# Kernel tuning notes

Hardware: AMD Instinct MI355X
Metric: run time of the kernel (lower is better)

Reference implementation:

```python
import jax, jax.numpy as jnp
import numpy as np

B, T, D, H, DK, DV = 2, 2048, 1024, 16, 64, 64
_MASK_ADDER = -10000.0  # tf-models MaskedSoftmax convention


def setup_inputs() -> dict:
    key = jax.random.key(0)
    ks = jax.random.split(key, 8)
    s = 0.02
    return {
        "query": jax.random.normal(ks[0], (B, T, D), jnp.float32),
        "value": jax.random.normal(ks[1], (B, T, D), jnp.float32),
        "Wq": jax.random.normal(ks[2], (D, H, DK), jnp.float32) * s,
        "bq": jnp.zeros((H, DK), jnp.float32),
        "Wk": jax.random.normal(ks[3], (D, H, DK), jnp.float32) * s,
        "bk": jnp.zeros((H, DK), jnp.float32),
        "Wv": jax.random.normal(ks[4], (D, H, DV), jnp.float32) * s,
        "bv": jnp.zeros((H, DV), jnp.float32),
        "Wo": jax.random.normal(ks[5], (H, DV, D), jnp.float32) * s,
        "bo": jnp.zeros((D,), jnp.float32),
        "attention_mask": jnp.ones((B, T, T), jnp.int32),
    }


def reference(query, value, Wq, bq, Wk, bk, Wv, bv, Wo, bo, attention_mask):
    # key defaults to value (call() with key=None); training=False -> no dropout
    q = jnp.einsum("btd,dhk->bthk", query, Wq) + bq          # [B,T,H,DK]
    k = jnp.einsum("bsd,dhk->bshk", value, Wk) + bk          # [B,S,H,DK]
    v = jnp.einsum("bsd,dhk->bshk", value, Wv) + bv          # [B,S,H,DV]
    q = q * (1.0 / jnp.sqrt(jnp.asarray(DK, q.dtype)))
    scores = jnp.einsum("bthk,bshk->bhts", q, k)             # [B,H,T,S]
    # MaskedSoftmax: expand mask at axis 1, additive -10000 on masked slots
    adder = (1.0 - attention_mask.astype(scores.dtype))[:, None, :, :] * _MASK_ADDER
    probs = jax.nn.softmax(scores + adder, axis=-1)
    ctx = jnp.einsum("bhts,bshv->bthv", probs, v)            # [B,T,H,DV]
    out = jnp.einsum("bthv,hvd->btd", ctx, Wo) + bo          # [B,T,D]
    return out
```

## Files before the change

kernel.cpp:

```cpp
#include <hip/hip_runtime.h>
#include <hip/hip_bf16.h>
#include <stdint.h>

#define TSEQ 2048
#define DMODEL 1024
#define NHEAD 16
#define HDIM 64
#define MROWS 4096
#define L2E 1.44269504088896340736f

typedef unsigned short u16;
typedef unsigned int u32;
typedef __attribute__((ext_vector_type(8))) short bf16x8;
typedef __attribute__((ext_vector_type(8))) unsigned short u16x8;
typedef __attribute__((ext_vector_type(4))) unsigned short u16x4;
typedef __attribute__((ext_vector_type(4))) float f32x4;
typedef __attribute__((ext_vector_type(16))) float f32x16;
typedef __attribute__((ext_vector_type(4))) unsigned int u32x4;

__device__ inline u16 f2bf(float f) {
  __hip_bfloat16 h(f);
  return __builtin_bit_cast(u16, h);
}

__device__ inline float fexp2(float x) { float r; asm("v_exp_f32 %0, %1" : "=v"(r) : "v"(x)); return r; }

__device__ inline unsigned cvtpk_bf16(float a, float b) {
  unsigned r; asm("v_cvt_pk_bf16_f32 %0, %1, %2" : "=v"(r) : "v"(a), "v"(b)); return r;
}

__device__ inline void permswap(u32& a, u32& b) {
  asm volatile("v_permlane32_swap_b32 %0, %1" : "+v"(a), "+v"(b));
}

__device__ inline void gload16(const void* g, void* l) {
  __builtin_amdgcn_global_load_lds((const __attribute__((address_space(1))) void*)g,
                                   (__attribute__((address_space(3))) void*)l, 16, 0, 0);
}

__global__ void prep(const float* __restrict__ q, const float* __restrict__ v,
                     u16* __restrict__ qo, u16* __restrict__ vo,
                     const float* __restrict__ Wq, const float* __restrict__ Wk,
                     const float* __restrict__ Wv, const float* __restrict__ Wo,
                     u16* __restrict__ WT3, u16* __restrict__ WoT,
                     const int* __restrict__ mask, int* __restrict__ flags) {
  __shared__ float tile[32][33];
  __shared__ int sred[4];
  const int bid = blockIdx.x, tid = threadIdx.x;
  if (bid < 8192) {
    const float* in = bid < 4096 ? q : v;
    u16* out = bid < 4096 ? qo : vo;
    const int i = (bid & 4095) * 1024 + tid * 4;
    float4 x = *(const float4*)(in + i);
    u16x4 o;
    o.x = f2bf(x.x); o.y = f2bf(x.y); o.z = f2bf(x.z); o.w = f2bf(x.w);
    *(u16x4*)(out + i) = o;
  } else if (bid < 12288) {
    int t = bid - 8192;
    const int z = t >> 10; t &= 1023;
    const float* W = z == 0 ? Wq : z == 1 ? Wk : z == 2 ? Wv : Wo;
    u16* WT = z < 3 ? (WT3 + (size_t)z * 1024 * 1024) : WoT;
    const int bx = t & 31, by = t >> 5;
    const int tr = tid >> 3;
    const int tc4 = (tid & 7) * 4;
    float4 x = *(const float4*)(W + (size_t)(by * 32 + tr) * 1024 + bx * 32 + tc4);
    tile[tr][tc4 + 0] = x.x; tile[tr][tc4 + 1] = x.y;
    tile[tr][tc4 + 2] = x.z; tile[tr][tc4 + 3] = x.w;
    __syncthreads();
    u16x4 o;
    o.x = f2bf(tile[tc4 + 0][tr]); o.y = f2bf(tile[tc4 + 1][tr]);
    o.z = f2bf(tile[tc4 + 2][tr]); o.w = f2bf(tile[tc4 + 3][tr]);
    *(u16x4*)(WT + (size_t)(bx * 32 + tr) * 1024 + by * 32 + tc4) = o;
  } else {
    const int t = bid - 12288;
    const int st = t & 15, qt = (t >> 4) & 15, b = t >> 8;
    const int row = qt * 128 + (tid >> 1);
    const int col0 = st * 128 + (tid & 1) * 64;
    const int* p = mask + (size_t)b * TSEQ * TSEQ + (size_t)row * TSEQ + col0;
    int ok = 1;
    #pragma unroll
    for (int j = 0; j < 64; j += 4) {
      int4 x = *(const int4*)(p + j);
      ok &= (x.x == 1) & (x.y == 1) & (x.z == 1) & (x.w == 1);
    }
    ok = __all(ok);
    if ((tid & 63) == 0) sred[tid >> 6] = ok;
    __syncthreads();
    if (tid == 0) flags[(b * 16 + qt) * 16 + st] = sred[0] & sred[1] & sred[2] & sred[3];
  }
}

__global__ __launch_bounds__(256) void gemm_qkv(
    const u16* __restrict__ qxb, const u16* __restrict__ vxb, const u16* __restrict__ WT3,
    const float* __restrict__ bq, const float* __restrict__ bk, const float* __restrict__ bv,
    u16* __restrict__ Qb, u16* __restrict__ Kb, u16* __restrict__ VTb, float qscale) {
  __shared__ u16 SMEM[64 * 64 + 128 * 64];
  u16* As = SMEM;
  u16* Bs = SMEM + 64 * 64;
  const int tid = threadIdx.x;
  const int w = tid >> 6, lane = tid & 63;
  const int lo = lane & 15, hi = lane >> 4;
  const int bid = blockIdx.x + (blockIdx.y << 6);
  const int swz = (bid & 7) * 192 + (bid >> 3);
  const int m0 = (swz & 63) << 6, n0 = (swz >> 6) << 7;
  const int nsel = n0 >> 10;
  const u16* A = nsel == 0 ? qxb : vxb;
  const float* bias = nsel == 0 ? bq : nsel == 1 ? bk : bv;
  const float scl = nsel == 0 ? qscale : 1.0f;
  const int wm = (w >> 1) * 32, wn = (w & 1) * 64;
  f32x4 acc[2][4] = {};
  for (int kt = 0; kt < 16; ++kt) {
    #pragma unroll
    for (int i = 0; i < 2; ++i) {
      const int off = tid * 16 + i * 4096;
      const int row = off >> 7;
      const int g = ((off >> 4) & 7) ^ (row & 7);
      gload16(A + (size_t)(m0 + row) * 1024 + kt * 64 + g * 8, (char*)As + off);
    }
    #pragma unroll
    for (int i = 0; i < 4; ++i) {
      const int off = tid * 16 + i * 4096;
      const int row = off >> 7;
      const int g = ((off >> 4) & 7) ^ (row & 7);
      gload16(WT3 + (size_t)(n0 + row) * 1024 + kt * 64 + g * 8, (char*)Bs + off);
    }
    __syncthreads();
    #pragma unroll
    for (int kk = 0; kk < 2; ++kk) {
      bf16x8 af[2], bfr[4];
      #pragma unroll
      for (int mi = 0; mi < 2; ++mi) {
        int row = wm + mi * 16 + lo;
        af[mi] = *(const bf16x8*)(As + row * 64 + (((kk * 4 + hi) ^ (row & 7)) << 3));
      }
      #pragma unroll
      for (int ni = 0; ni < 4; ++ni) {
        int row = wn + ni * 16 + lo;
        bfr[ni] = *(const bf16x8*)(Bs + row * 64 + (((kk * 4 + hi) ^ (row & 7)) << 3));
      }
      #pragma unroll
      for (int mi = 0; mi < 2; ++mi)
        #pragma unroll
        for (int ni = 0; ni < 4; ++ni)
          acc[mi][ni] = __builtin_amdgcn_mfma_f32_16x16x32_bf16(af[mi], bfr[ni], acc[mi][ni], 0, 0, 0);
    }
    __syncthreads();
  }
  if (nsel < 2) {
    u16* dst = nsel == 0 ? Qb : Kb;
    #pragma unroll
    for (int ni = 0; ni < 4; ++ni) {
      const int col = (n0 + wn + ni * 16 + lo) & 1023;
      const float bc = bias[col];
      #pragma unroll
      for (int mi = 0; mi < 2; ++mi) {
        #pragma unroll
        for (int r = 0; r < 4; ++r) {
          const int row = m0 + wm + mi * 16 + hi * 4 + r;
          const float v = (acc[mi][ni][r] + bc) * scl;
          dst[(size_t)(((row >> 11) * NHEAD + (col >> 6)) * TSEQ + (row & 2047)) * HDIM + (col & 63)] = f2bf(v);
        }
      }
    }
  } else {
    u16* T = SMEM;
    __syncthreads();
    #pragma unroll
    for (int ni = 0; ni < 4; ++ni) {
      const int nl = wn + ni * 16 + lo;
      const float bc = bias[(n0 + nl) & 1023];
      #pragma unroll
      for (int mi = 0; mi < 2; ++mi) {
        const int mloc = wm + mi * 16 + hi * 4;
        u16x4 pk;
        #pragma unroll
        for (int r = 0; r < 4; ++r) pk[r] = f2bf(acc[mi][ni][r] + bc);
        const int cg = mloc >> 3;
        *(u16x4*)(T + nl * 64 + (((cg ^ (nl & 7)) << 3) + (mloc & 7))) = pk;
      }
    }
    __syncthreads();
    const int b_ = m0 >> 11, t0_ = m0 & 2047;
    #pragma unroll
    for (int j = 0; j < 4; ++j) {
      const int c = tid + j * 256;
      const int nl = c >> 3;
      const int cg0 = c & 7;
      u16x8 val = *(const u16x8*)(T + nl * 64 + ((cg0 ^ (nl & 7)) << 3));
      const int colg = (n0 + nl) & 1023;
      u16* dst = VTb + ((size_t)(b_ * NHEAD + (colg >> 6)) * 64 + (colg & 63)) * TSEQ + t0_ + cg0 * 8;
      *(u16x8*)dst = val;
    }
  }
}

__global__ __launch_bounds__(256) void gemm_o(const u16* __restrict__ A, const u16* __restrict__ BT,
                                              const float* __restrict__ bias, float* __restrict__ C) {
  __shared__ u16 As[64 * 64];
  __shared__ u16 Bs[64 * 64];
  const int tid = threadIdx.x;
  const int w = tid >> 6, lane = tid & 63;
  const int lo = lane & 15, hi = lane >> 4;
  const int bid = blockIdx.x + (blockIdx.y << 6);
  const int swz = (bid & 7) * 128 + (bid >> 3);
  const int m0 = (swz & 63) << 6, n0 = (swz >> 6) << 6;
  const int wm = (w >> 1) * 32, wn = (w & 1) * 32;
  f32x4 acc[2][2] = {};
  for (int kt = 0; kt < 16; ++kt) {
    #pragma unroll
    for (int i = 0; i < 2; ++i) {
      const int off = tid * 16 + i * 4096;
      const int row = off >> 7;
      const int g = ((off >> 4) & 7) ^ (row & 7);
      gload16(A + (size_t)(m0 + row) * 1024 + kt * 64 + g * 8, (char*)As + off);
      gload16(BT + (size_t)(n0 + row) * 1024 + kt * 64 + g * 8, (char*)Bs + off);
    }
    __syncthreads();
    #pragma unroll
    for (int kk = 0; kk < 2; ++kk) {
      bf16x8 af[2], bfr[2];
      #pragma unroll
      for (int mi = 0; mi < 2; ++mi) {
        int row = wm + mi * 16 + lo;
        af[mi] = *(const bf16x8*)(As + row * 64 + (((kk * 4 + hi) ^ (row & 7)) << 3));
      }
      #pragma unroll
      for (int ni = 0; ni < 2; ++ni) {
        int row = wn + ni * 16 + lo;
        bfr[ni] = *(const bf16x8*)(Bs + row * 64 + (((kk * 4 + hi) ^ (row & 7)) << 3));
      }
      #pragma unroll
      for (int mi = 0; mi < 2; ++mi)
        #pragma unroll
        for (int ni = 0; ni < 2; ++ni)
          acc[mi][ni] = __builtin_amdgcn_mfma_f32_16x16x32_bf16(af[mi], bfr[ni], acc[mi][ni], 0, 0, 0);
    }
    __syncthreads();
  }
  #pragma unroll
  for (int ni = 0; ni < 2; ++ni) {
    const int col = n0 + wn + ni * 16 + lo;
    const float bc = bias[col];
    #pragma unroll
    for (int mi = 0; mi < 2; ++mi)
      #pragma unroll
      for (int r = 0; r < 4; ++r) {
        const int row = m0 + wm + mi * 16 + hi * 4 + r;
        C[(size_t)row * DMODEL + col] = acc[mi][ni][r] + bc;
      }
  }
}

__global__ __launch_bounds__(256) void flash(
    const u16* __restrict__ Q, const u16* __restrict__ K, const u16* __restrict__ VT,
    const int* __restrict__ mask, const int* __restrict__ flags, u16* __restrict__ ctx) {
  __shared__ u16 Ks[2][64 * 64];
  __shared__ u16 Vs[3][64 * 64];
  const int tid = threadIdx.x, w = tid >> 6, lane = tid & 63;
  const int l5 = lane & 31, hi2 = lane >> 5;
  const int bid0 = blockIdx.x + (blockIdx.y << 4);
  const int swz = (bid0 & 7) * 64 + (bid0 >> 3);
  const int qt = swz & 15, bh = swz >> 4;
  const int b = bh >> 4, h = bh & 15;
  const int tq = qt * 128 + w * 32;

  const int soff = w * 2048 + lane * 16;
  const int srow0 = w * 16 + (lane >> 3);
  const int lg0 = (((lane & 7) ^ (lane >> 3) ^ ((w * 2) & 3)) << 3);
  const int lg1 = (((lane & 7) ^ (lane >> 3) ^ ((w * 2 + 1) & 3)) << 3);

  bf16x8 qf[4];
  #pragma unroll
  for (int kc = 0; kc < 4; ++kc)
    qf[kc] = *(const bf16x8*)(Q + ((size_t)bh * TSEQ + tq + l5) * 64 + kc * 16 + hi2 * 8);

  unsigned fl = 0;
  {
    const int* fp = flags + (b * 16 + qt) * 16;
    #pragma unroll
    for (int i = 0; i < 4; ++i) {
      int4 v = *(const int4*)(fp + i * 4);
      fl |= (unsigned)((v.x & 1) | ((v.y & 1) << 1) | ((v.z & 1) << 2) | ((v.w & 1) << 3)) << (4 * i);
    }
  }

  f32x16 o0 = {}, o1 = {};
  float lrow = 0.f;
  bf16x8 paA[4], paB[4];

#define STAGE_K(buf, st_) do {                                                        \
    const u16* kb_ = K + ((size_t)bh * TSEQ + (st_) * 64) * 64;                       \
    gload16(kb_ + (size_t)srow0 * 64 + lg0, (char*)Ks[buf] + soff);                   \
    gload16(kb_ + (size_t)(srow0 + 8) * 64 + lg1, (char*)Ks[buf] + soff + 1024);      \
  } while (0)
#define STAGE_V(buf, st_) do {                                                        \
    const u16* vb_ = VT + (size_t)bh * 64 * TSEQ + (st_) * 64;                        \
    gload16(vb_ + (size_t)srow0 * TSEQ + lg0, (char*)Vs[buf] + soff);                 \
    gload16(vb_ + (size_t)(srow0 + 8) * TSEQ + lg1, (char*)Vs[buf] + soff + 1024);    \
  } while (0)

#define FR(base, row, sg) \
  (*(const bf16x8*)((base) + (row) * 64 + ((((sg) ^ ((row) & 7) ^ (((row) >> 3) & 3)) << 3))))

#define QKC(T, S0, S1) do {                                                           \
    const u16* Kb_ = Ks[(T) & 1];                                                     \
    _Pragma("unroll") for (int kc = 0; kc < 4; ++kc) {                                \
      const int sg = kc * 2 + hi2;                                                    \
      S0 = __builtin_amdgcn_mfma_f32_32x32x16_bf16(FR(Kb_, l5, sg), qf[kc], S0, 0, 0, 0); \
      S1 = __builtin_amdgcn_mfma_f32_32x32x16_bf16(FR(Kb_, 32 + l5, sg), qf[kc], S1, 0, 0, 0); \
    } } while (0)

#define PVC(VB, PA) do {                                                              \
    const u16* Vb_ = Vs[VB];                                                          \
    _Pragma("unroll") for (int kc = 0; kc < 4; ++kc) {                                \
      const int sg = kc * 2 + hi2;                                                    \
      o0 = __builtin_amdgcn_mfma_f32_32x32x16_bf16(PA[kc], FR(Vb_, l5, sg), o0, 0, 0, 0); \
      o1 = __builtin_amdgcn_mfma_f32_32x32x16_bf16(PA[kc], FR(Vb_, 32 + l5, sg), o1, 0, 0, 0); \
    } } while (0)

#define SMAX(T, S0, S1, PAOUT) do {                                                   \
    if (!((fl >> ((T) >> 1)) & 1)) {                                                  \
      const int t_ = tq + l5;                                                         \
      const int* mp_ = mask + ((size_t)b * TSEQ + t_) * TSEQ + (T) * 64;              \
      _Pragma("unroll") for (int r = 0; r < 16; ++r) {                                \
        const int sr_ = (r & 3) + 8 * (r >> 2) + 4 * hi2;                             \
        S0[r] += (1.0f - (float)mp_[sr_]) * -14426.950408f;                           \
        S1[r] += (1.0f - (float)mp_[sr_ + 32]) * -14426.950408f;                      \
      } }                                                                             \
    float rs = 0.f; u32 W0_[8], W1_[8];                                               \
    _Pragma("unroll") for (int q_ = 0; q_ < 4; ++q_)                                  \
      _Pragma("unroll") for (int c_ = 0; c_ < 2; ++c_) {                              \
        const int r = 4 * q_ + 2 * c_;                                                \
        float a0 = fexp2(S0[r]), b0 = fexp2(S0[r + 1]);                               \
        float a1 = fexp2(S1[r]), b1 = fexp2(S1[r + 1]);                               \
        rs += (a0 + b0) + (a1 + b1);                                                  \
        W0_[q_ * 2 + c_] = cvtpk_bf16(a0, b0);                                        \
        W1_[q_ * 2 + c_] = cvtpk_bf16(a1, b1); }                                      \
    rs += __shfl_xor(rs, 32); lrow += rs;                                             \
    _Pragma("unroll") for (int ts = 0; ts < 2; ++ts)                                  \
      _Pragma("unroll") for (int qp = 0; qp < 2; ++qp) {                              \
        u32 d0 = ts ? W1_[(2 * qp) * 2 + 0] : W0_[(2 * qp) * 2 + 0];                  \
        u32 e0 = ts ? W1_[(2 * qp + 1) * 2 + 0] : W0_[(2 * qp + 1) * 2 + 0];          \
        u32 d1 = ts ? W1_[(2 * qp) * 2 + 1] : W0_[(2 * qp) * 2 + 1];                  \
        u32 e1 = ts ? W1_[(2 * qp + 1) * 2 + 1] : W0_[(2 * qp + 1) * 2 + 1];          \
        permswap(d0, e0); permswap(d1, e1);                                           \
        u32x4 fw_; fw_.x = d0; fw_.y = d1; fw_.z = e0; fw_.w = e1;                    \
        PAOUT[ts * 2 + qp] = __builtin_bit_cast(bf16x8, fw_); }                       \
  } while (0)

#define BODY(T, VPREV, VNEXT, DOSTAGE, PAIN, PAOUT) do {                              \
    if (DOSTAGE) { STAGE_K(((T) + 1) & 1, (T) + 1); STAGE_V(VNEXT, (T) + 1); }        \
    f32x16 s0 = {}, s1 = {};                                                          \
    __builtin_amdgcn_s_setprio(1);                                                    \
    QKC(T, s0, s1);                                                                   \
    PVC(VPREV, PAIN);                                                                 \
    __builtin_amdgcn_s_setprio(0);                                                    \
    SMAX(T, s0, s1, PAOUT);                                                           \
    __syncthreads();                                                                  \
  } while (0)

  STAGE_K(0, 0); STAGE_V(0, 0);
  __syncthreads();
  {
    f32x16 s0 = {}, s1 = {};
    __builtin_amdgcn_s_setprio(1);
    QKC(0, s0, s1);
    __builtin_amdgcn_s_setprio(0);
    STAGE_K(1, 1); STAGE_V(1, 1);
    SMAX(0, s0, s1, paA);
    __syncthreads();
  }

  int vp = 0, vn = 2;
  for (int t = 1; t < 31; t += 2) {
    BODY(t, vp, vn, 1, paA, paB);
    const int vp2 = (vp + 1 == 3) ? 0 : vp + 1;
    const int vn2 = (vn + 1 == 3) ? 0 : vn + 1;
    BODY(t + 1, vp2, vn2, 1, paB, paA);
    vp = (vp2 + 1 == 3) ? 0 : vp2 + 1;
    vn = (vn2 + 1 == 3) ? 0 : vn2 + 1;
  }
  BODY(31, vp, 0, 0, paA, paB);

  __builtin_amdgcn_s_setprio(1);
  PVC(1, paB);
  __builtin_amdgcn_s_setprio(0);

#undef BODY
#undef SMAX
#undef PVC
#undef QKC
#undef FR
#undef STAGE_V
#undef STAGE_K

  const float inv = 1.0f / lrow;
  #pragma unroll
  for (int r = 0; r < 16; ++r) {
    const int sr = (r & 3) + 8 * (r >> 2) + 4 * hi2;
    const float ir = __shfl(inv, sr);
    u16* cp = ctx + (size_t)(b * TSEQ + tq + sr) * DMODEL + h * 64;
    cp[l5] = f2bf(o0[r] * ir);
    cp[32 + l5] = f2bf(o1[r] * ir);
  }
}

extern "C" void kernel_launch(void* const* d_in, const int* in_sizes, int n_in,
                              void* d_out, int out_size, void* d_ws, size_t ws_size,
                              hipStream_t stream) {
  (void)in_sizes; (void)n_in; (void)out_size; (void)ws_size;
  const float* query = (const float*)d_in[0];
  const float* value = (const float*)d_in[1];
  const float* Wq = (const float*)d_in[2];
  const float* bq = (const float*)d_in[3];
  const float* Wk = (const float*)d_in[4];
  const float* bk = (const float*)d_in[5];
  const float* Wv = (const float*)d_in[6];
  const float* bv = (const float*)d_in[7];
  const float* Wo = (const float*)d_in[8];
  const float* bo = (const float*)d_in[9];
  const int* amask = (const int*)d_in[10];

  char* ws = (char*)d_ws;
  const size_t MB = 1 << 20;
  u16* qxb = (u16*)(ws + 0 * MB);
  u16* vxb = (u16*)(ws + 8 * MB);
  u16* WT3 = (u16*)(ws + 16 * MB);
  u16* Qb  = (u16*)(ws + 24 * MB);
  u16* Kb  = (u16*)(ws + 32 * MB);
  int* flg = (int*)(ws + 42 * MB);
  u16* WoT = (u16*)(ws + 44 * MB);
  u16* VTb = (u16*)(ws + 48 * MB);
  u16* ctx = (u16*)(ws + 56 * MB);

  prep<<<12800, 256, 0, stream>>>(query, value, qxb, vxb, Wq, Wk, Wv, Wo, WT3, WoT, amask, flg);
  gemm_qkv<<<dim3(64, 24), 256, 0, stream>>>(qxb, vxb, WT3, bq, bk, bv, Qb, Kb, VTb, 0.125f * L2E);
  flash<<<dim3(16, 32), 256, 0, stream>>>(Qb, Kb, VTb, amask, flg, ctx);
  gemm_o<<<dim3(64, 16), 256, 0, stream>>>(ctx, WoT, bo, (float*)d_out);
}
```

Baseline: 136.0 us.

## Process two KV tiles per barrier with deeper K/V shared-memory ring buffers

Enlarges the K and V shared-memory buffers from 2/3 to 4/5 slots and restructures the flash loop so each iteration stages two future tiles and computes two QK/softmax/PV steps before a single __syncthreads. This halves the number of block-wide barriers and gives the async loads more time to land ahead of use. In exchange, LDS per block grows from 40KB to 72KB, which can reduce how many blocks fit per CU, and the buffer-index rotation logic is more involved.

```diff
diff --git a/kernel.cpp b/kernel.cpp
--- a/kernel.cpp
+++ b/kernel.cpp
@@ -254,8 +254,8 @@
 __global__ __launch_bounds__(256) void flash(
     const u16* __restrict__ Q, const u16* __restrict__ K, const u16* __restrict__ VT,
     const int* __restrict__ mask, const int* __restrict__ flags, u16* __restrict__ ctx) {
-  __shared__ u16 Ks[2][64 * 64];
-  __shared__ u16 Vs[3][64 * 64];
+  __shared__ u16 Ks[4][64 * 64];
+  __shared__ u16 Vs[5][64 * 64];
   const int tid = threadIdx.x, w = tid >> 6, lane = tid & 63;
   const int l5 = lane & 31, hi2 = lane >> 5;
   const int bid0 = blockIdx.x + (blockIdx.y << 4);
@@ -302,8 +302,8 @@
 #define FR(base, row, sg) \
   (*(const bf16x8*)((base) + (row) * 64 + ((((sg) ^ ((row) & 7) ^ (((row) >> 3) & 3)) << 3))))
 
-#define QKC(T, S0, S1) do {                                                           \
-    const u16* Kb_ = Ks[(T) & 1];                                                     \
+#define QKC(KB, S0, S1) do {                                                          \
+    const u16* Kb_ = Ks[KB];                                                          \
     _Pragma("unroll") for (int kc = 0; kc < 4; ++kc) {                                \
       const int sg = kc * 2 + hi2;                                                    \
       S0 = __builtin_amdgcn_mfma_f32_32x32x16_bf16(FR(Kb_, l5, sg), qf[kc], S0, 0, 0, 0); \
@@ -348,45 +348,58 @@
         PAOUT[ts * 2 + qp] = __builtin_bit_cast(bf16x8, fw_); }                       \
   } while (0)
 
-#define BODY(T, VPREV, VNEXT, DOSTAGE, PAIN, PAOUT) do {                              \
-    if (DOSTAGE) { STAGE_K(((T) + 1) & 1, (T) + 1); STAGE_V(VNEXT, (T) + 1); }        \
-    f32x16 s0 = {}, s1 = {};                                                          \
-    __builtin_amdgcn_s_setprio(1);                                                    \
-    QKC(T, s0, s1);                                                                   \
-    PVC(VPREV, PAIN);                                                                 \
-    __builtin_amdgcn_s_setprio(0);                                                    \
-    SMAX(T, s0, s1, PAOUT);                                                           \
-    __syncthreads();                                                                  \
-  } while (0)
-
-  STAGE_K(0, 0); STAGE_V(0, 0);
+  STAGE_K(0, 0); STAGE_K(1, 1); STAGE_V(0, 0); STAGE_V(1, 1);
   __syncthreads();
+
   {
+    STAGE_K(2, 2); STAGE_K(3, 3); STAGE_V(2, 2); STAGE_V(3, 3);
     f32x16 s0 = {}, s1 = {};
     __builtin_amdgcn_s_setprio(1);
     QKC(0, s0, s1);
     __builtin_amdgcn_s_setprio(0);
-    STAGE_K(1, 1); STAGE_V(1, 1);
-    SMAX(0, s0, s1, paA);
-    __syncthreads();
-  }
-
-  int vp = 0, vn = 2;
-  for (int t = 1; t < 31; t += 2) {
-    BODY(t, vp, vn, 1, paA, paB);
-    const int vp2 = (vp + 1 == 3) ? 0 : vp + 1;
-    const int vn2 = (vn + 1 == 3) ? 0 : vn + 1;
-    BODY(t + 1, vp2, vn2, 1, paB, paA);
-    vp = (vp2 + 1 == 3) ? 0 : vp2 + 1;
-    vn = (vn2 + 1 == 3) ? 0 : vn2 + 1;
-  }
-  BODY(31, vp, 0, 0, paA, paB);
+    SMAX(0, s0, s1, paB);
+    f32x16 u0 = {}, u1 = {};
+    __builtin_amdgcn_s_setprio(1);
+    QKC(1, u0, u1);
+    PVC(0, paB);
+    __builtin_amdgcn_s_setprio(0);
+    SMAX(1, u0, u1, paA);
+    __syncthreads();
+  }
+
+  int kA = 2, kB = 3;
+  int vA = 1, vB = 2;
+  int vC = 4, vD = 0;
+  for (int j = 1; j < 16; ++j) {
+    const int T0 = 2 * j;
+    if (j < 15) {
+      STAGE_K(kA ^ 2, T0 + 2); STAGE_K(kB ^ 2, T0 + 3);
+      STAGE_V(vC, T0 + 2); STAGE_V(vD, T0 + 3);
+    }
+    f32x16 s0 = {}, s1 = {};
+    __builtin_amdgcn_s_setprio(1);
+    QKC(kA, s0, s1);
+    PVC(vA, paA);
+    __builtin_amdgcn_s_setprio(0);
+    SMAX(T0, s0, s1, paB);
+    f32x16 u0 = {}, u1 = {};
+    __builtin_amdgcn_s_setprio(1);
+    QKC(kB, u0, u1);
+    PVC(vB, paB);
+    __builtin_amdgcn_s_setprio(0);
+    SMAX(T0 + 1, u0, u1, paA);
+    __syncthreads();
+    kA ^= 2; kB ^= 2;
+    vA += 2; if (vA >= 5) vA -= 5;
+    vB += 2; if (vB >= 5) vB -= 5;
+    vC += 2; if (vC >= 5) vC -= 5;
+    vD += 2; if (vD >= 5) vD -= 5;
+  }
 
   __builtin_amdgcn_s_setprio(1);
-  PVC(1, paB);
+  PVC(1, paA);
   __builtin_amdgcn_s_setprio(0);
 
-#undef BODY
 #undef SMAX
 #undef PVC
 #undef QKC
```

New measurement: 139.1 us. +2.3%, slower.
